# Optimization experiments

Measured on AMD Instinct MI355X. Metric: run time of the kernel, lower is better.

The kernel has to match this reference:

```python
import jax, jax.numpy as jnp
import numpy as np

# Constants from init_kwargs
NODE_BUDGET = 200.0
ALPHA = 0.5
COS_EPS = 1e-6

N, F = 200000, 256   # num_nodes, num_features
B = 1024             # batch_size (roots)
M = 500000           # candidate (u, batch) pairs this hop
E = 2000000          # frontier->candidate edges


def setup_inputs() -> dict:
    key = jax.random.key(0)
    ks = jax.random.split(key, 12)
    bound = 1.0 / np.sqrt(F)
    return {
        "x": jax.random.normal(ks[0], (N, F), dtype=jnp.float32),
        "w_ego_root": jax.random.uniform(ks[1], (F,), minval=-bound, maxval=bound, dtype=jnp.float32),
        "w_ego_u": jax.random.uniform(ks[2], (F,), minval=-bound, maxval=bound, dtype=jnp.float32),
        "w_layer_v": jax.random.uniform(ks[3], (F,), minval=-bound, maxval=bound, dtype=jnp.float32),
        "w_layer_u": jax.random.uniform(ks[4], (F,), minval=-bound, maxval=bound, dtype=jnp.float32),
        "n_imp": jax.random.uniform(ks[5], (N,), dtype=jnp.float32),
        "budgets": jnp.ones((B,), dtype=jnp.float32) * NODE_BUDGET,
        "batch_nodes": jax.random.randint(ks[6], (B,), 0, N, dtype=jnp.int32),
        "u_ids": jax.random.randint(ks[7], (M,), 0, N, dtype=jnp.int32),
        "batch_ptr": jnp.sort(jax.random.randint(ks[8], (M,), 0, B, dtype=jnp.int32)),
        "edge_src": jax.random.randint(ks[9], (E,), 0, B, dtype=jnp.int32),
        "edge_dst": jax.random.randint(ks[10], (E,), 0, M, dtype=jnp.int32),
    }


def reference(x, w_ego_root, w_ego_u, w_layer_v, w_layer_u, n_imp, budgets,
              batch_nodes, u_ids, batch_ptr, edge_src, edge_dst):
    # One hop of AdaptiveSampler.batch_wise_sampling score computation.
    # h_roots = x[batch_nodes] * w_ego_root  -> [B, F]
    x_roots = x[batch_nodes]                       # [B, F] gather
    h_roots = x_roots * w_ego_root                 # [B, F]
    xu = x[u_ids]                                  # [M, F] gather (dominant traffic)
    hu = xu * w_ego_u                              # [M, F]
    hr = h_roots[batch_ptr]                        # [M, F] gather

    # ego_score = cosine(h_roots[batch_ptr], x[u] * w_ego_u)
    dot = jnp.sum(hr * hu, axis=-1)                # [M]
    nr = jnp.linalg.norm(hr, axis=-1)
    nu = jnp.linalg.norm(hu, axis=-1)
    ego_score = dot / (jnp.maximum(nr, COS_EPS) * jnp.maximum(nu, COS_EPS))

    # layer_kernel: frontier projection scattered onto candidates via adjacency,
    # combined with the candidate projection (assumed tanh combine; see notes).
    sv = x_roots @ w_layer_v                       # [B]
    agg = jax.ops.segment_sum(sv[edge_src], edge_dst, num_segments=M)  # [M]
    su = xu @ w_layer_u                            # [M]
    layer_score = jnp.tanh(agg + su)               # [M]

    # p_u = (a*ego + (1-a)*layer) * n_imp[u] * (budget/node_budget)
    p_u = (ALPHA * ego_score + (1.0 - ALPHA) * layer_score) \
          * n_imp[u_ids] * (budgets[batch_ptr] / NODE_BUDGET)

    # per-batch normalizer (detached in original: .clone().detach())
    p_norm = jax.lax.stop_gradient(
        jax.ops.segment_max(p_u, batch_ptr, num_segments=B))  # [B]
    p_u = p_u / p_norm[batch_ptr] + 1.0
    # replace_nan(p_u, nan_to=0.0, inf_to=1.0)
    p_u = jnp.where(jnp.isnan(p_u), 0.0, jnp.where(jnp.isinf(p_u), 1.0, p_u))
    # p_clip = clamp(p_u, 1e-5, 1)
    p_clip = jnp.clip(p_u, 1e-5, 1.0)
    return p_clip
```

## Files before the change

### kernel.cpp

```cpp
#include <hip/hip_runtime.h>

#define F 256
#define NODE_BUDGET 200.0f
#define COS_EPS 1e-6f

__global__ __launch_bounds__(256) void root_kernel(
    const float* __restrict__ x,
    const float* __restrict__ w_ego_root,
    const float* __restrict__ w_ego_u,
    const float* __restrict__ w_layer_v,
    const float* __restrict__ budgets,
    const int* __restrict__ batch_nodes,
    float* __restrict__ g, float* __restrict__ nr,
    float* __restrict__ sv, float* __restrict__ bscale)
{
    __shared__ float red[2][4];
    int b = blockIdx.x;
    int f = threadIdx.x;
    int root = batch_nodes[b];
    float xf = x[(size_t)root * F + f];
    float hr = xf * w_ego_root[f];
    g[(size_t)b * F + f] = hr * w_ego_u[f];
    float a = hr * hr;
    float c = xf * w_layer_v[f];
    #pragma unroll
    for (int off = 32; off; off >>= 1) {
        a += __shfl_xor(a, off);
        c += __shfl_xor(c, off);
    }
    int lane = f & 63, wv = f >> 6;
    if (lane == 0) { red[0][wv] = a; red[1][wv] = c; }
    __syncthreads();
    if (f == 0) {
        float as = red[0][0] + red[0][1] + red[0][2] + red[0][3];
        float cs = red[1][0] + red[1][1] + red[1][2] + red[1][3];
        nr[b] = sqrtf(as);
        sv[b] = cs;
        bscale[b] = budgets[b] * (1.0f / NODE_BUDGET);
    }
}

__global__ __launch_bounds__(256) void edge_kernel(
    const int* __restrict__ edge_src, const int* __restrict__ edge_dst,
    const float* __restrict__ sv, float* __restrict__ agg, int E)
{
    int i = blockIdx.x * 256 + threadIdx.x;
    int stride = gridDim.x * 256;
    for (; i < E; i += stride)
        atomicAdd(&agg[edge_dst[i]], sv[edge_src[i]]);
}

__global__ __launch_bounds__(256) void cand_kernel(
    const float* __restrict__ x,
    const float* __restrict__ w_ego_u,
    const float* __restrict__ w_layer_u,
    const float* __restrict__ n_imp,
    const int* __restrict__ u_ids, const int* __restrict__ batch_ptr,
    const float* __restrict__ g, const float* __restrict__ nr,
    const float* __restrict__ bscale, const float* __restrict__ agg,
    float* __restrict__ p_out, int M)
{
    int gid = blockIdx.x * 256 + threadIdx.x;
    int m = gid >> 6;
    int lane = gid & 63;
    if (m >= M) return;
    int u = u_ids[m];
    int b = batch_ptr[m];
    float4 xs = ((const float4*)(x + (size_t)u * F))[lane];
    float4 gv = ((const float4*)(g + (size_t)b * F))[lane];
    float4 wu = ((const float4*)w_ego_u)[lane];
    float4 wl = ((const float4*)w_layer_u)[lane];
    float d = xs.x * gv.x + xs.y * gv.y + xs.z * gv.z + xs.w * gv.w;
    float h0 = xs.x * wu.x, h1 = xs.y * wu.y, h2 = xs.z * wu.z, h3 = xs.w * wu.w;
    float n2 = h0 * h0 + h1 * h1 + h2 * h2 + h3 * h3;
    float s = xs.x * wl.x + xs.y * wl.y + xs.z * wl.z + xs.w * wl.w;
    #pragma unroll
    for (int off = 32; off; off >>= 1) {
        d  += __shfl_xor(d, off);
        n2 += __shfl_xor(n2, off);
        s  += __shfl_xor(s, off);
    }
    if (lane == 0) {
        float nu = sqrtf(n2);
        float ego = d / (fmaxf(nr[b], COS_EPS) * fmaxf(nu, COS_EPS));
        float layer = tanhf(agg[m] + s);
        float p = (0.5f * ego + 0.5f * layer) * n_imp[u] * bscale[b];
        p_out[m] = p;
    }
}

__global__ __launch_bounds__(256) void segmax_kernel(
    const float* __restrict__ p, const int* __restrict__ batch_ptr,
    float* __restrict__ pmax, int M)
{
    int b = blockIdx.x;
    int lo = 0, hi = M;
    while (lo < hi) { int mid = (lo + hi) >> 1; if (batch_ptr[mid] < b) lo = mid + 1; else hi = mid; }
    int start = lo;
    hi = M;
    while (lo < hi) { int mid = (lo + hi) >> 1; if (batch_ptr[mid] <= b) lo = mid + 1; else hi = mid; }
    int end = lo;
    float mx = -INFINITY;
    for (int i = start + threadIdx.x; i < end; i += 256)
        mx = fmaxf(mx, p[i]);
    #pragma unroll
    for (int off = 32; off; off >>= 1)
        mx = fmaxf(mx, __shfl_xor(mx, off));
    __shared__ float red[4];
    int lane = threadIdx.x & 63, wv = threadIdx.x >> 6;
    if (lane == 0) red[wv] = mx;
    __syncthreads();
    if (threadIdx.x == 0)
        pmax[b] = fmaxf(fmaxf(red[0], red[1]), fmaxf(red[2], red[3]));
}

__global__ __launch_bounds__(256) void fin_kernel(
    const float* __restrict__ pmax,
    const int* __restrict__ batch_ptr, float* __restrict__ out, int M)
{
    int m = blockIdx.x * 256 + threadIdx.x;
    if (m >= M) return;
    float p = out[m];
    float pn = pmax[batch_ptr[m]];
    float v = p / pn + 1.0f;
    if (isnan(v)) v = 0.0f;
    else if (isinf(v)) v = 1.0f;
    v = fminf(fmaxf(v, 1e-5f), 1.0f);
    out[m] = v;
}

extern "C" void kernel_launch(void* const* d_in, const int* in_sizes, int n_in,
                              void* d_out, int out_size, void* d_ws, size_t ws_size,
                              hipStream_t stream) {
    const float* x          = (const float*)d_in[0];
    const float* w_ego_root = (const float*)d_in[1];
    const float* w_ego_u    = (const float*)d_in[2];
    const float* w_layer_v  = (const float*)d_in[3];
    const float* w_layer_u  = (const float*)d_in[4];
    const float* n_imp      = (const float*)d_in[5];
    const float* budgets    = (const float*)d_in[6];
    const int* batch_nodes = (const int*)d_in[7];
    const int* u_ids       = (const int*)d_in[8];
    const int* batch_ptr   = (const int*)d_in[9];
    const int* edge_src    = (const int*)d_in[10];
    const int* edge_dst    = (const int*)d_in[11];
    float* out = (float*)d_out;

    int B = in_sizes[7];
    int M = in_sizes[8];
    int E = in_sizes[10];

    float* ws = (float*)d_ws;
    size_t off = 0;
    float* agg = ws + off;                          off += (size_t)((M + 3) & ~3);
    size_t zero_bytes = off * sizeof(float);
    float* pmax   = ws + off;                       off += (size_t)((B + 3) & ~3);
    float* g      = ws + off;                       off += (size_t)B * F;
    float* nr     = ws + off;                       off += (size_t)((B + 3) & ~3);
    float* sv     = ws + off;                       off += (size_t)((B + 3) & ~3);
    float* bscale = ws + off;                       off += (size_t)((B + 3) & ~3);

    hipMemsetAsync(d_ws, 0, zero_bytes, stream);

    root_kernel<<<B, 256, 0, stream>>>(x, w_ego_root, w_ego_u, w_layer_v,
                                       budgets, batch_nodes, g, nr, sv, bscale);
    edge_kernel<<<2048, 256, 0, stream>>>(edge_src, edge_dst, sv, agg, E);
    int cand_blocks = (M + 3) / 4;
    cand_kernel<<<cand_blocks, 256, 0, stream>>>(x, w_ego_u, w_layer_u, n_imp,
                                                 u_ids, batch_ptr, g, nr, bscale,
                                                 agg, out, M);
    segmax_kernel<<<B, 256, 0, stream>>>(out, batch_ptr, pmax, M);
    fin_kernel<<<(M + 255) / 256, 256, 0, stream>>>(pmax, batch_ptr, out, M);
}
```

Measured before the change: 548.6 us.

## Precompute per-node norm/projection table, shrink candidate work, fuse segmax with normalize

Adds a pass over all N nodes that computes each node's ego norm, layer projection and n_imp into a float4 table. The candidate kernel then only needs one dot product per pair, processed by 16 lanes instead of a full wavefront. The segment max and final normalization are fused into one kernel. The cost is an extra streaming read of all of x (N=200k rows versus M=500k random gathers), though that read is coalesced and the table lookups replace redundant per-candidate reductions.

```diff
diff --git a/kernel.cpp b/kernel.cpp
--- a/kernel.cpp
+++ b/kernel.cpp
@@ -40,6 +40,32 @@
     }
 }
 
+__global__ __launch_bounds__(256) void nodes_kernel(
+    const float* __restrict__ x,
+    const float* __restrict__ w_ego_u,
+    const float* __restrict__ w_layer_u,
+    const float* __restrict__ n_imp,
+    float4* __restrict__ nodetab, int N)
+{
+    int wv = (blockIdx.x * 256 + threadIdx.x) >> 6;
+    int lane = threadIdx.x & 63;
+    if (wv >= N) return;
+    const float4* xr = (const float4*)(x + (size_t)wv * F);
+    float4 xv = xr[lane];
+    float4 wu = ((const float4*)w_ego_u)[lane];
+    float4 wl = ((const float4*)w_layer_u)[lane];
+    float h0 = xv.x * wu.x, h1 = xv.y * wu.y, h2 = xv.z * wu.z, h3 = xv.w * wu.w;
+    float a = h0 * h0 + h1 * h1 + h2 * h2 + h3 * h3;
+    float s = xv.x * wl.x + xv.y * wl.y + xv.z * wl.z + xv.w * wl.w;
+    #pragma unroll
+    for (int off = 32; off; off >>= 1) {
+        a += __shfl_xor(a, off);
+        s += __shfl_xor(s, off);
+    }
+    if (lane == 0)
+        nodetab[wv] = make_float4(sqrtf(a), s, n_imp[wv], 0.0f);
+}
+
 __global__ __launch_bounds__(256) void edge_kernel(
     const int* __restrict__ edge_src, const int* __restrict__ edge_dst,
     const float* __restrict__ sv, float* __restrict__ agg, int E)
@@ -52,46 +78,43 @@
 
 __global__ __launch_bounds__(256) void cand_kernel(
     const float* __restrict__ x,
-    const float* __restrict__ w_ego_u,
-    const float* __restrict__ w_layer_u,
-    const float* __restrict__ n_imp,
     const int* __restrict__ u_ids, const int* __restrict__ batch_ptr,
     const float* __restrict__ g, const float* __restrict__ nr,
     const float* __restrict__ bscale, const float* __restrict__ agg,
+    const float4* __restrict__ nodetab,
     float* __restrict__ p_out, int M)
 {
-    int gid = blockIdx.x * 256 + threadIdx.x;
-    int m = gid >> 6;
-    int lane = gid & 63;
+    int tid = threadIdx.x;
+    int lane = tid & 63;
+    int sub = lane >> 4;
+    int sl = lane & 15;
+    int m = blockIdx.x * 16 + (tid >> 6) * 4 + sub;
     if (m >= M) return;
     int u = u_ids[m];
     int b = batch_ptr[m];
-    float4 xs = ((const float4*)(x + (size_t)u * F))[lane];
-    float4 gv = ((const float4*)(g + (size_t)b * F))[lane];
-    float4 wu = ((const float4*)w_ego_u)[lane];
-    float4 wl = ((const float4*)w_layer_u)[lane];
-    float d = xs.x * gv.x + xs.y * gv.y + xs.z * gv.z + xs.w * gv.w;
-    float h0 = xs.x * wu.x, h1 = xs.y * wu.y, h2 = xs.z * wu.z, h3 = xs.w * wu.w;
-    float n2 = h0 * h0 + h1 * h1 + h2 * h2 + h3 * h3;
-    float s = xs.x * wl.x + xs.y * wl.y + xs.z * wl.z + xs.w * wl.w;
+    const float4* xr = (const float4*)(x + (size_t)u * F);
+    const float4* gr = (const float4*)(g + (size_t)b * F);
+    float acc = 0.0f;
     #pragma unroll
-    for (int off = 32; off; off >>= 1) {
-        d  += __shfl_xor(d, off);
-        n2 += __shfl_xor(n2, off);
-        s  += __shfl_xor(s, off);
+    for (int p = 0; p < 4; ++p) {
+        float4 xv = xr[p * 16 + sl];
+        float4 gv = gr[p * 16 + sl];
+        acc += xv.x * gv.x + xv.y * gv.y + xv.z * gv.z + xv.w * gv.w;
     }
-    if (lane == 0) {
-        float nu = sqrtf(n2);
-        float ego = d / (fmaxf(nr[b], COS_EPS) * fmaxf(nu, COS_EPS));
-        float layer = tanhf(agg[m] + s);
-        float p = (0.5f * ego + 0.5f * layer) * n_imp[u] * bscale[b];
+    #pragma unroll
+    for (int off = 8; off; off >>= 1)
+        acc += __shfl_xor(acc, off);
+    if (sl == 0) {
+        float4 nv = nodetab[u];
+        float ego = acc / (fmaxf(nr[b], COS_EPS) * fmaxf(nv.x, COS_EPS));
+        float layer = tanhf(agg[m] + nv.y);
+        float p = (0.5f * ego + 0.5f * layer) * nv.z * bscale[b];
         p_out[m] = p;
     }
 }
 
-__global__ __launch_bounds__(256) void segmax_kernel(
-    const float* __restrict__ p, const int* __restrict__ batch_ptr,
-    float* __restrict__ pmax, int M)
+__global__ __launch_bounds__(256) void seg_norm_kernel(
+    const int* __restrict__ batch_ptr, float* __restrict__ out, int M)
 {
     int b = blockIdx.x;
     int lo = 0, hi = M;
@@ -102,31 +125,25 @@
     int end = lo;
     float mx = -INFINITY;
     for (int i = start + threadIdx.x; i < end; i += 256)
-        mx = fmaxf(mx, p[i]);
+        mx = fmaxf(mx, out[i]);
     #pragma unroll
     for (int off = 32; off; off >>= 1)
         mx = fmaxf(mx, __shfl_xor(mx, off));
     __shared__ float red[4];
+    __shared__ float s_pn;
     int lane = threadIdx.x & 63, wv = threadIdx.x >> 6;
     if (lane == 0) red[wv] = mx;
     __syncthreads();
     if (threadIdx.x == 0)
-        pmax[b] = fmaxf(fmaxf(red[0], red[1]), fmaxf(red[2], red[3]));
-}
-
-__global__ __launch_bounds__(256) void fin_kernel(
-    const float* __restrict__ pmax,
-    const int* __restrict__ batch_ptr, float* __restrict__ out, int M)
-{
-    int m = blockIdx.x * 256 + threadIdx.x;
-    if (m >= M) return;
-    float p = out[m];
-    float pn = pmax[batch_ptr[m]];
-    float v = p / pn + 1.0f;
-    if (isnan(v)) v = 0.0f;
-    else if (isinf(v)) v = 1.0f;
-    v = fminf(fmaxf(v, 1e-5f), 1.0f);
-    out[m] = v;
+        s_pn = fmaxf(fmaxf(red[0], red[1]), fmaxf(red[2], red[3]));
+    __syncthreads();
+    float pn = s_pn;
+    for (int i = start + threadIdx.x; i < end; i += 256) {
+        float v = out[i] / pn + 1.0f;
+        if (isnan(v)) v = 0.0f;
+        else if (isinf(v)) v = 1.0f;
+        out[i] = fminf(fmaxf(v, 1e-5f), 1.0f);
+    }
 }
 
 extern "C" void kernel_launch(void* const* d_in, const int* in_sizes, int n_in,
@@ -146,6 +163,7 @@
     const int* edge_dst    = (const int*)d_in[11];
     float* out = (float*)d_out;
 
+    int N = in_sizes[5];
     int B = in_sizes[7];
     int M = in_sizes[8];
     int E = in_sizes[10];
@@ -154,21 +172,20 @@
     size_t off = 0;
     float* agg = ws + off;                          off += (size_t)((M + 3) & ~3);
     size_t zero_bytes = off * sizeof(float);
-    float* pmax   = ws + off;                       off += (size_t)((B + 3) & ~3);
-    float* g      = ws + off;                       off += (size_t)B * F;
-    float* nr     = ws + off;                       off += (size_t)((B + 3) & ~3);
-    float* sv     = ws + off;                       off += (size_t)((B + 3) & ~3);
-    float* bscale = ws + off;                       off += (size_t)((B + 3) & ~3);
+    float* g       = ws + off;                      off += (size_t)B * F;
+    float* nr      = ws + off;                      off += (size_t)((B + 3) & ~3);
+    float* sv      = ws + off;                      off += (size_t)((B + 3) & ~3);
+    float* bscale  = ws + off;                      off += (size_t)((B + 3) & ~3);
+    float4* nodetab = (float4*)(ws + off);          off += (size_t)N * 4;
 
     hipMemsetAsync(d_ws, 0, zero_bytes, stream);
 
     root_kernel<<<B, 256, 0, stream>>>(x, w_ego_root, w_ego_u, w_layer_v,
                                        budgets, batch_nodes, g, nr, sv, bscale);
+    nodes_kernel<<<(N + 3) / 4, 256, 0, stream>>>(x, w_ego_u, w_layer_u, n_imp,
+                                                  nodetab, N);
     edge_kernel<<<2048, 256, 0, stream>>>(edge_src, edge_dst, sv, agg, E);
-    int cand_blocks = (M + 3) / 4;
-    cand_kernel<<<cand_blocks, 256, 0, stream>>>(x, w_ego_u, w_layer_u, n_imp,
-                                                 u_ids, batch_ptr, g, nr, bscale,
-                                                 agg, out, M);
-    segmax_kernel<<<B, 256, 0, stream>>>(out, batch_ptr, pmax, M);
-    fin_kernel<<<(M + 255) / 256, 256, 0, stream>>>(pmax, batch_ptr, out, M);
+    cand_kernel<<<(M + 15) / 16, 256, 0, stream>>>(x, u_ids, batch_ptr, g, nr,
+                                                   bscale, agg, nodetab, out, M);
+    seg_norm_kernel<<<B, 256, 0, stream>>>(batch_ptr, out, M);
 }
```

Result: faster. 487.6 us (-11.1%).
